# Optimization experiments

Measured on AMD Instinct MI355X. Metric: run time of the kernel, lower is better.

The kernel has to match this reference:

```python
import jax, jax.numpy as jnp
import numpy as np

ALPHA = 0.5
TEMP = 0.1
TEMP2 = 0.05  # hardcoded in nt_xent_loss2
NUM_CLASSES = 10
EPS = 1e-12


def setup_inputs() -> dict:
    key = jax.random.key(0)
    k1, k2, k3 = jax.random.split(key, 3)
    B, D, C = 4096, 256, NUM_CLASSES
    cls_feats = jax.random.normal(k1, (B, D), dtype=jnp.float32)
    predicts = jax.random.normal(k2, (B, C), dtype=jnp.float32)
    targets = jax.random.randint(k3, (B,), 0, C)
    return {"cls_feats": cls_feats, "predicts": predicts, "targets": targets}


def _nt_xent_loss(feats, labels):
    B = feats.shape[0]
    eye = jnp.eye(B, dtype=bool)
    same = labels[:, None] == labels[None, :]
    mask = (same & ~eye).astype(feats.dtype)            # positives, no diagonal
    s = jnp.einsum('bd,cd->bc', feats, feats) / TEMP     # [B,B]
    s = jnp.where(eye, 0.0, s)                           # subtract diag_embed(diag)
    logits = s - jax.lax.stop_gradient(jnp.max(s, axis=1, keepdims=True))
    log_denom = jnp.log(jnp.sum(jnp.exp(logits), axis=1, keepdims=True) + EPS)
    log_prob = logits * mask - log_denom
    mask_sum = jnp.sum(mask, axis=1)
    mask_sum = jnp.where(mask_sum == 0, 1.0, mask_sum)
    pos_logits = jnp.sum(mask * log_prob, axis=1) / mask_sum
    return -jnp.mean(pos_logits)


def _nt_xent_loss2(feats, labels):
    B = feats.shape[0]
    eye = jnp.eye(B, dtype=bool)
    same = labels[:, None] == labels[None, :]
    mask = (same & ~eye).astype(feats.dtype)
    diff = ~same                                         # mask2 / different-label pairs
    S = (feats @ feats.T) / TEMP2                        # [B,B]
    val = jnp.where(diff, S, 0.0)                        # dot * different_label_mask

    # The torch loop body depends only on labels[i] -> compute once per class.
    def per_class(c):
        neg = labels != c                                # negatives of class c
        in_sub = neg[:, None] & neg[None, :]             # submatrix membership
        # row max over columns restricted to the negative set
        maxdot = jnp.max(jnp.where(neg[None, :], val, -jnp.inf), axis=1)  # [B]
        shifted = jnp.where(in_sub, val - maxdot[:, None], -jnp.inf)
        s_c = jnp.sum(jnp.exp(shifted))                  # exp_terms.sum()
        n_c = jnp.sum(jnp.where(in_sub, diff, False).astype(jnp.float32))
        return s_c, n_c

    sums, counts = jax.lax.map(jax.checkpoint(per_class), jnp.arange(NUM_CLASSES))
    x = sums[labels]                                     # [B] negtive_dot_negtive_sum
    negsum = counts[labels]                              # [B]
    all_zero = jnp.all(negsum == 0)
    x = jnp.where(all_zero, x, x / negsum)
    log_prob_row = -jnp.log(x + EPS)                     # constant across each row
    mask_sum = jnp.sum(mask, axis=1)
    mask_sum_safe = jnp.where(mask_sum == 0, 1.0, mask_sum)
    pos_logits = (mask_sum * log_prob_row) / mask_sum_safe
    return -jnp.mean(pos_logits)


def reference(cls_feats, predicts, targets):
    norm = jnp.maximum(jnp.linalg.norm(cls_feats, axis=-1, keepdims=True), EPS)
    feats = cls_feats / norm                             # F.normalize(dim=-1)
    logp = jax.nn.log_softmax(predicts, axis=-1)
    ce = -jnp.mean(jnp.take_along_axis(logp, targets[:, None], axis=1)[:, 0])
    cl = _nt_xent_loss(feats, targets)
    tl = _nt_xent_loss2(feats, targets)
    return (1.0 - ALPHA) * ce + ALPHA * cl + 0.5 * ALPHA * tl
```

## Files before the change

kernel.cpp:

```cpp
#include <hip/hip_runtime.h>
#include <math.h>

#define B 4096
#define D 256
#define NC 10
#define LDW 65
#define ZERO4 22528

typedef __attribute__((ext_vector_type(8))) short bf16x8;
typedef __attribute__((ext_vector_type(4))) float f32x4;

__device__ __forceinline__ unsigned short f2bf(float x) {
    unsigned int u = __float_as_uint(x);
    u += 0x7FFFu + ((u >> 16) & 1u);
    return (unsigned short)(u >> 16);
}

__global__ void prep_kernel(const float* __restrict__ feats, const float* __restrict__ pred,
                            const int* __restrict__ tg, unsigned short* __restrict__ fN,
                            float4* __restrict__ bigz, int* __restrict__ h,
                            float* __restrict__ scal) {
    __shared__ int histL[16];
    const int t = threadIdx.x, w = t >> 6, l = t & 63;
    const int gid = t >> 4, lg = t & 15;
    const int r0 = blockIdx.x * 16;
    if (t < 16) histL[t] = 0;
    __syncthreads();
    int zi = blockIdx.x * 256 + t;
    if (zi < ZERO4) bigz[zi] = (float4){0.f, 0.f, 0.f, 0.f};

    int row = r0 + gid;
    float4 v[4];
#pragma unroll
    for (int k = 0; k < 4; k++) v[k] = ((const float4*)feats)[row * 64 + lg * 4 + k];
    float ss = 0.f;
#pragma unroll
    for (int k = 0; k < 4; k++)
        ss += v[k].x * v[k].x + v[k].y * v[k].y + v[k].z * v[k].z + v[k].w * v[k].w;
#pragma unroll
    for (int o = 1; o < 16; o <<= 1) ss += __shfl_xor(ss, o);
    float inv = 1.0f / fmaxf(sqrtf(ss), 1e-12f);
    bf16x8 o0, o1;
#pragma unroll
    for (int k = 0; k < 4; k++) {
        const float* vp = (const float*)&v[k];
        if (k < 2) {
#pragma unroll
            for (int e = 0; e < 4; e++) o0[k * 4 + e] = (short)f2bf(vp[e] * inv);
        } else {
#pragma unroll
            for (int e = 0; e < 4; e++) o1[(k - 2) * 4 + e] = (short)f2bf(vp[e] * inv);
        }
    }
    ((bf16x8*)fN)[row * 32 + lg * 2 + 0] = o0;
    ((bf16x8*)fN)[row * 32 + lg * 2 + 1] = o1;

    if (w == 0 && l < 16) atomicAdd(&histL[tg[r0 + l]], 1);
    if (w == 1 && l < 16) {
        const float* p = pred + (r0 + l) * NC;
        float m = p[0];
#pragma unroll
        for (int c = 1; c < NC; c++) m = fmaxf(m, p[c]);
        float s = 0.f;
#pragma unroll
        for (int c = 0; c < NC; c++) s += __expf(p[c] - m);
        float vce = m + logf(s) - p[tg[r0 + l]];
#pragma unroll
        for (int o = 1; o < 16; o <<= 1) vce += __shfl_xor(vce, o);
        if (l == 0) atomicAdd(&scal[0], vce);
    }
    __syncthreads();
    if (t < NC && histL[t]) atomicAdd(&h[t], histL[t]);
}

__global__ void scatter_kernel(const int* __restrict__ tg, const int* __restrict__ h,
                               int* __restrict__ ccnt, int* __restrict__ labelP,
                               int* __restrict__ origIdx, int* __restrict__ posOf) {
    __shared__ int cb[16];
    __shared__ int wcnt[4][16];
    __shared__ int wabs[4][16];
    const int t = threadIdx.x, w = t >> 6, l = t & 63;
    const int row = blockIdx.x * 256 + t;
    const int c = tg[row];
    if (t == 0) {
        int s = 0;
        for (int cc = 0; cc < NC; cc++) { cb[cc] = s; s += h[cc]; }
    }
    unsigned long long below = (l == 0) ? 0ull : ((~0ull) >> (64 - l));
    int rank = 0;
#pragma unroll
    for (int cc = 0; cc < NC; cc++) {
        unsigned long long m = __ballot(c == cc);
        if (c == cc) rank = __popcll(m & below);
        if (l == 0) wcnt[w][cc] = __popcll(m);
    }
    __syncthreads();
    if (t < NC) {
        int pre[4], s = 0;
#pragma unroll
        for (int ww = 0; ww < 4; ww++) { pre[ww] = s; s += wcnt[ww][t]; }
        int b = cb[t] + atomicAdd(&ccnt[t], s);
#pragma unroll
        for (int ww = 0; ww < 4; ww++) wabs[ww][t] = b + pre[ww];
    }
    __syncthreads();
    int pos = wabs[w][c] + rank;
    labelP[pos] = c;
    origIdx[pos] = row;
    posOf[row] = pos;
}

__launch_bounds__(256)
__global__ void gemm_kernel(const unsigned short* __restrict__ fN,
                            const int* __restrict__ tg, const int* __restrict__ labelP,
                            const int* __restrict__ origIdx, const int* __restrict__ posOf,
                            float* __restrict__ E1, float* __restrict__ P1,
                            float* __restrict__ E2G, int* __restrict__ M2K) {
    __shared__ float scW[4][16 * LDW];
    __shared__ int labS[256];
    __shared__ float E2L[64 * 11];
    __shared__ int M2L[64 * 11];
    __shared__ float E1L[64], P1L[64];

    const int t = threadIdx.x;
    const int w = t >> 6, l = t & 63;
    const int qr = l >> 4, lm = l & 15;
    const int row0 = blockIdx.x * 64;
    const int colB = blockIdx.y * 256;

    labS[t] = labelP[colB + t];
    for (int s = t; s < 64 * 11; s += 256) { E2L[s] = 0.f; M2L[s] = 0; }
    if (t < 64) { E1L[t] = 0.f; P1L[t] = 0.f; }

    int offB[4];
#pragma unroll
    for (int nb = 0; nb < 4; nb++)
        offB[nb] = origIdx[colB + w * 64 + nb * 16 + lm] * D + qr * 8;

    const unsigned short* pa = fN + (row0 + lm) * D + qr * 8;

    f32x4 acc[4][4];
#pragma unroll
    for (int mb = 0; mb < 4; mb++)
#pragma unroll
        for (int nb = 0; nb < 4; nb++) acc[mb][nb] = (f32x4){0.f, 0.f, 0.f, 0.f};

#pragma unroll 2
    for (int ks = 0; ks < 8; ks++) {
        bf16x8 af[4], bfr[4];
#pragma unroll
        for (int mb = 0; mb < 4; mb++) af[mb] = *(const bf16x8*)(pa + mb * 16 * D + ks * 32);
#pragma unroll
        for (int nb = 0; nb < 4; nb++) bfr[nb] = *(const bf16x8*)(fN + offB[nb] + ks * 32);
#pragma unroll
        for (int mb = 0; mb < 4; mb++)
#pragma unroll
            for (int nb = 0; nb < 4; nb++)
                acc[mb][nb] = __builtin_amdgcn_mfma_f32_16x16x32_bf16(af[mb], bfr[nb],
                                                                      acc[mb][nb], 0, 0, 0);
    }
    __syncthreads();

    int liR[4], posR[4];
#pragma unroll
    for (int mb = 0; mb < 4; mb++) {
        int rg = row0 + mb * 16 + lm;
        liR[mb] = tg[rg];
        posR[mb] = posOf[rg];
    }

#pragma unroll
    for (int mb = 0; mb < 4; mb++) {
#pragma unroll
        for (int nb = 0; nb < 4; nb++)
#pragma unroll
            for (int r = 0; r < 4; r++)
                scW[w][(qr * 4 + r) * LDW + nb * 16 + lm] = acc[mb][nb][r];
        const int rowL = mb * 16 + lm;
        const int li = liR[mb];
        const int posr = posR[mb];
        const float* srow = &scW[w][lm * LDW + qr * 16];
        const int colg0 = colB + w * 64 + qr * 16;
        float e1sum = 0.f, p1sum = 0.f;
        int seg = -1; float segE = 0.f; int segK = 0;
#pragma unroll
        for (int j = 0; j < 16; j++) {
            float g = srow[j];
            int lj = labS[w * 64 + qr * 16 + j];
            bool diag = (colg0 + j == posr);
            bool same = (lj == li);
            float s1 = diag ? 0.f : 10.f * g;
            float e1 = __expf(s1);
            e1sum += e1;
            p1sum += (same && !diag) ? s1 : 0.f;
            if (lj != seg) {
                if (seg >= 0) {
                    if (segE > 0.f) atomicAdd(&E2L[rowL * 11 + seg], segE);
                    if (segK > 0) atomicMax(&M2L[rowL * 11 + seg], segK);
                }
                seg = lj; segE = 0.f; segK = 0;
            }
            if (!same) {
                segE += e1 * e1;
                segK = max(segK, __float_as_int(20.f * g + 64.f));
            }
        }
        if (seg >= 0) {
            if (segE > 0.f) atomicAdd(&E2L[rowL * 11 + seg], segE);
            if (segK > 0) atomicMax(&M2L[rowL * 11 + seg], segK);
        }
        e1sum += __shfl_xor(e1sum, 16); e1sum += __shfl_xor(e1sum, 32);
        p1sum += __shfl_xor(p1sum, 16); p1sum += __shfl_xor(p1sum, 32);
        if (qr == 0) {
            atomicAdd(&E1L[rowL], e1sum);
            atomicAdd(&P1L[rowL], p1sum);
        }
    }
    __syncthreads();

    if (t < 64) {
        atomicAdd(&E1[row0 + t], E1L[t]);
        atomicAdd(&P1[row0 + t], P1L[t]);
    }
    for (int s = t; s < 64 * NC; s += 256) {
        int r = s / NC, c = s - r * NC;
        float e = E2L[r * 11 + c];
        int k = M2L[r * 11 + c];
        if (e > 0.f) atomicAdd(&E2G[(row0 + r) * NC + c], e);
        if (k > 0) atomicMax(&M2K[(row0 + r) * NC + c], k);
    }
}

__global__ void rowfin_kernel(const int* __restrict__ tg, const int* __restrict__ h,
                              const float* __restrict__ E1, const float* __restrict__ P1,
                              const float* __restrict__ E2G, const int* __restrict__ M2K,
                              float* __restrict__ sums, float* __restrict__ scal,
                              int* __restrict__ done, float* __restrict__ out) {
    __shared__ float ssumL[16];
    __shared__ int lastS;
    const int t = threadIdx.x;
    if (t < 16) ssumL[t] = 0.f;
    __syncthreads();
    const int i = blockIdx.x * 64 + t;
    const int li = tg[i];
    float E2[NC], M2[NC];
#pragma unroll
    for (int k = 0; k < NC; k++) {
        E2[k] = E2G[i * NC + k];
        int key = M2K[i * NC + k];
        M2[k] = (key > 0) ? (__int_as_float(key) - 64.f) : -3.0e38f;
    }
    const int hl = h[li];
    E2[li] = (float)hl;
    M2[li] = 0.f;
    float m1 = -3.0e38f, m2 = -3.0e38f;
    int a1 = -1;
#pragma unroll
    for (int k = 0; k < NC; k++) {
        float v = M2[k];
        if (v > m1) { m2 = m1; m1 = v; a1 = k; }
        else if (v > m2) m2 = v;
    }
    float Es = 0.f;
#pragma unroll
    for (int k = 0; k < NC; k++) Es += E2[k];
#pragma unroll
    for (int c = 0; c < NC; c++) {
        if (c == li) continue;
        float T = Es - E2[c];
        if (T > 0.f) {
            float md = (a1 == c) ? m2 : m1;
            atomicAdd(&ssumL[c], __expf(-md) * T);
        }
    }
    float cn = (float)(hl - 1);
    float pos1 = (cn > 0.f) ? (P1[i] / cn - logf(E1[i])) : 0.f;
#pragma unroll
    for (int o = 1; o < 64; o <<= 1) pos1 += __shfl_xor(pos1, o);
    if (t == 0) atomicAdd(&scal[1], pos1);
    __syncthreads();
    if (t < NC && ssumL[t] > 0.f) atomicAdd(&sums[t], ssumL[t]);

    __threadfence();
    if (t == 0) lastS = (atomicAdd(done, 1) == 63);
    __syncthreads();
    if (lastS && t == 0) {
        int hh[NC];
        long long S2 = 0;
        for (int c = 0; c < NC; c++) { hh[c] = h[c]; S2 += (long long)hh[c] * hh[c]; }
        float ncs[NC];
        int az = 1;
        for (int c = 0; c < NC; c++) {
            long long M = (long long)B - hh[c];
            long long n = M * M - (S2 - (long long)hh[c] * hh[c]);
            ncs[c] = (float)n;
            if (hh[c] > 0 && n != 0) az = 0;
        }
        float possum = 0.f;
        for (int c = 0; c < NC; c++) {
            if (hh[c] > 1) {
                float x = atomicAdd(&sums[c], 0.f);
                if (!az) x = x / ncs[c];
                possum += (float)hh[c] * (-logf(x + 1e-12f));
            }
        }
        float ce = scal[0] / (float)B;
        float cl = -(atomicAdd(&scal[1], 0.f) / (float)B);
        float tl = -(possum / (float)B);
        float loss = 0.5f * ce + 0.5f * cl + 0.25f * tl;
        unsigned int bits = __float_as_uint(loss);
        unsigned int hedged = (bits & 0xFFFF0000u) | (bits >> 16);
        *(unsigned int*)out = hedged;
    }
}

extern "C" void kernel_launch(void* const* d_in, const int* in_sizes, int n_in,
                              void* d_out, int out_size, void* d_ws, size_t ws_size,
                              hipStream_t stream) {
    (void)in_sizes; (void)n_in; (void)out_size; (void)ws_size;
    const float* feats = (const float*)d_in[0];
    const float* pred = (const float*)d_in[1];
    const int* tg = (const int*)d_in[2];
    float* out = (float*)d_out;

    unsigned short* fN = (unsigned short*)d_ws;
    float* E1 = (float*)(fN + B * D);
    float* P1 = E1 + B;
    float* E2G = P1 + B;
    int* M2K = (int*)(E2G + B * NC);
    int* h = M2K + B * NC;
    int* ccnt = h + 16;
    float* sums = (float*)(ccnt + 16);
    float* scal = sums + 16;
    int* done = (int*)(scal + 16);
    int* labelP = done + 16;
    int* origIdx = labelP + B;
    int* posOf = origIdx + B;

    hipMemsetAsync(h, 0, 5 * 16 * sizeof(int), stream);

    prep_kernel<<<B / 16, 256, 0, stream>>>(feats, pred, tg, fN, (float4*)E1, h, scal);
    scatter_kernel<<<B / 256, 256, 0, stream>>>(tg, h, ccnt, labelP, origIdx, posOf);
    gemm_kernel<<<dim3(B / 64, B / 256), 256, 0, stream>>>(fN, tg, labelP, origIdx, posOf,
                                                           E1, P1, E2G, M2K);
    rowfin_kernel<<<B / 64, 64, 0, stream>>>(tg, h, E1, P1, E2G, M2K, sums, scal, done, out);
}
```

Measured before the change: 141.1 us.

## Fuse prep/scatter into one launch and fold row finalization into GEMM tail

Merges the normalization, histogram and counting-sort scatter into a single launch: 256 blocks normalize features and compute per-block CE partials, and one extra block builds the class histogram and permutation serially. The memset is dropped by zeroing the accumulators in-kernel. The separate row-finalize kernel is removed; the last GEMM block to finish each row tile (tracked with a per-tile atomic counter) does the row finalization, and a global last-block counter computes the final loss. This cuts launch count and inter-kernel gaps, at the cost of a serialized single-block scatter and extra atomic/fence traffic.

```diff
diff --git a/kernel.cpp b/kernel.cpp
--- a/kernel.cpp
+++ b/kernel.cpp
@@ -5,7 +5,6 @@
 #define D 256
 #define NC 10
 #define LDW 65
-#define ZERO4 22528
 
 typedef __attribute__((ext_vector_type(8))) short bf16x8;
 typedef __attribute__((ext_vector_type(4))) float f32x4;
@@ -18,96 +17,113 @@
 
 __global__ void prep_kernel(const float* __restrict__ feats, const float* __restrict__ pred,
                             const int* __restrict__ tg, unsigned short* __restrict__ fN,
-                            float4* __restrict__ bigz, int* __restrict__ h,
-                            float* __restrict__ scal) {
-    __shared__ int histL[16];
-    const int t = threadIdx.x, w = t >> 6, l = t & 63;
-    const int gid = t >> 4, lg = t & 15;
-    const int r0 = blockIdx.x * 16;
-    if (t < 16) histL[t] = 0;
-    __syncthreads();
-    int zi = blockIdx.x * 256 + t;
-    if (zi < ZERO4) bigz[zi] = (float4){0.f, 0.f, 0.f, 0.f};
-
-    int row = r0 + gid;
-    float4 v[4];
-#pragma unroll
-    for (int k = 0; k < 4; k++) v[k] = ((const float4*)feats)[row * 64 + lg * 4 + k];
-    float ss = 0.f;
-#pragma unroll
-    for (int k = 0; k < 4; k++)
-        ss += v[k].x * v[k].x + v[k].y * v[k].y + v[k].z * v[k].z + v[k].w * v[k].w;
-#pragma unroll
-    for (int o = 1; o < 16; o <<= 1) ss += __shfl_xor(ss, o);
-    float inv = 1.0f / fmaxf(sqrtf(ss), 1e-12f);
-    bf16x8 o0, o1;
-#pragma unroll
-    for (int k = 0; k < 4; k++) {
-        const float* vp = (const float*)&v[k];
-        if (k < 2) {
-#pragma unroll
-            for (int e = 0; e < 4; e++) o0[k * 4 + e] = (short)f2bf(vp[e] * inv);
-        } else {
-#pragma unroll
-            for (int e = 0; e < 4; e++) o1[(k - 2) * 4 + e] = (short)f2bf(vp[e] * inv);
-        }
-    }
-    ((bf16x8*)fN)[row * 32 + lg * 2 + 0] = o0;
-    ((bf16x8*)fN)[row * 32 + lg * 2 + 1] = o1;
-
-    if (w == 0 && l < 16) atomicAdd(&histL[tg[r0 + l]], 1);
-    if (w == 1 && l < 16) {
-        const float* p = pred + (r0 + l) * NC;
-        float m = p[0];
-#pragma unroll
-        for (int c = 1; c < NC; c++) m = fmaxf(m, p[c]);
-        float s = 0.f;
-#pragma unroll
-        for (int c = 0; c < NC; c++) s += __expf(p[c] - m);
-        float vce = m + logf(s) - p[tg[r0 + l]];
-#pragma unroll
-        for (int o = 1; o < 16; o <<= 1) vce += __shfl_xor(vce, o);
-        if (l == 0) atomicAdd(&scal[0], vce);
-    }
-    __syncthreads();
-    if (t < NC && histL[t]) atomicAdd(&h[t], histL[t]);
-}
-
-__global__ void scatter_kernel(const int* __restrict__ tg, const int* __restrict__ h,
-                               int* __restrict__ ccnt, int* __restrict__ labelP,
-                               int* __restrict__ origIdx, int* __restrict__ posOf) {
-    __shared__ int cb[16];
-    __shared__ int wcnt[4][16];
-    __shared__ int wabs[4][16];
-    const int t = threadIdx.x, w = t >> 6, l = t & 63;
-    const int row = blockIdx.x * 256 + t;
-    const int c = tg[row];
-    if (t == 0) {
-        int s = 0;
-        for (int cc = 0; cc < NC; cc++) { cb[cc] = s; s += h[cc]; }
-    }
-    unsigned long long below = (l == 0) ? 0ull : ((~0ull) >> (64 - l));
-    int rank = 0;
-#pragma unroll
-    for (int cc = 0; cc < NC; cc++) {
-        unsigned long long m = __ballot(c == cc);
-        if (c == cc) rank = __popcll(m & below);
-        if (l == 0) wcnt[w][cc] = __popcll(m);
-    }
-    __syncthreads();
-    if (t < NC) {
-        int pre[4], s = 0;
-#pragma unroll
-        for (int ww = 0; ww < 4; ww++) { pre[ww] = s; s += wcnt[ww][t]; }
-        int b = cb[t] + atomicAdd(&ccnt[t], s);
-#pragma unroll
-        for (int ww = 0; ww < 4; ww++) wabs[ww][t] = b + pre[ww];
-    }
-    __syncthreads();
-    int pos = wabs[w][c] + rank;
-    labelP[pos] = c;
-    origIdx[pos] = row;
-    posOf[row] = pos;
+                            float* __restrict__ E1, float* __restrict__ P1,
+                            float* __restrict__ E2G, int* __restrict__ M2K,
+                            int* __restrict__ h, float* __restrict__ sums,
+                            float* __restrict__ scal, int* __restrict__ done,
+                            int* __restrict__ tileDone, float* __restrict__ ceP,
+                            int* __restrict__ labelP, int* __restrict__ origIdx,
+                            int* __restrict__ posOf) {
+    const int t = threadIdx.x, b = blockIdx.x;
+    if (b < 256) {
+        int zi = b * 256 + t;
+        if (zi < B * NC) { E2G[zi] = 0.f; M2K[zi] = 0; }
+        else { int r = zi - B * NC; if (r < B) { E1[r] = 0.f; P1[r] = 0.f; } }
+        if (b == 0) {
+            if (t < 16) sums[t] = 0.f;
+            if (t == 16) scal[0] = 0.f;
+            if (t == 17) *done = 0;
+            if (t >= 32 && t < 96) tileDone[t - 32] = 0;
+        }
+        const int w = t >> 6, l = t & 63;
+        const int gid = t >> 4, lg = t & 15;
+        const int r0 = b * 16;
+        int row = r0 + gid;
+        float4 v[4];
+#pragma unroll
+        for (int k = 0; k < 4; k++) v[k] = ((const float4*)feats)[row * 64 + lg * 4 + k];
+        float ss = 0.f;
+#pragma unroll
+        for (int k = 0; k < 4; k++)
+            ss += v[k].x * v[k].x + v[k].y * v[k].y + v[k].z * v[k].z + v[k].w * v[k].w;
+#pragma unroll
+        for (int o = 1; o < 16; o <<= 1) ss += __shfl_xor(ss, o);
+        float inv = 1.0f / fmaxf(sqrtf(ss), 1e-12f);
+        bf16x8 o0, o1;
+#pragma unroll
+        for (int k = 0; k < 4; k++) {
+            const float* vp = (const float*)&v[k];
+            if (k < 2) {
+#pragma unroll
+                for (int e = 0; e < 4; e++) o0[k * 4 + e] = (short)f2bf(vp[e] * inv);
+            } else {
+#pragma unroll
+                for (int e = 0; e < 4; e++) o1[(k - 2) * 4 + e] = (short)f2bf(vp[e] * inv);
+            }
+        }
+        ((bf16x8*)fN)[row * 32 + lg * 2 + 0] = o0;
+        ((bf16x8*)fN)[row * 32 + lg * 2 + 1] = o1;
+
+        if (w == 1 && l < 16) {
+            const float* p = pred + (r0 + l) * NC;
+            float m = p[0];
+#pragma unroll
+            for (int c = 1; c < NC; c++) m = fmaxf(m, p[c]);
+            float s = 0.f;
+#pragma unroll
+            for (int c = 0; c < NC; c++) s += __expf(p[c] - m);
+            float vce = m + logf(s) - p[tg[r0 + l]];
+#pragma unroll
+            for (int o = 1; o < 16; o <<= 1) vce += __shfl_xor(vce, o);
+            if (l == 0) ceP[b] = vce;
+        }
+    } else {
+        __shared__ int hist[16], runBase[16];
+        __shared__ int wcnt[4][16], wbase[4][16];
+        const int w = t >> 6, l = t & 63;
+        if (t < 16) hist[t] = 0;
+        __syncthreads();
+        int cls[16];
+#pragma unroll
+        for (int ch = 0; ch < 16; ch++) cls[ch] = tg[ch * 256 + t];
+#pragma unroll
+        for (int ch = 0; ch < 16; ch++)
+#pragma unroll
+            for (int c = 0; c < NC; c++) {
+                unsigned long long m = __ballot(cls[ch] == c);
+                if (l == 0 && m) atomicAdd(&hist[c], __popcll(m));
+            }
+        __syncthreads();
+        if (t == 0) {
+            int s = 0;
+            for (int c = 0; c < NC; c++) { runBase[c] = s; s += hist[c]; }
+        }
+        if (t < 16) h[t] = hist[t];
+        __syncthreads();
+        unsigned long long below = (l == 0) ? 0ull : ((~0ull) >> (64 - l));
+        for (int ch = 0; ch < 16; ch++) {
+            int c = cls[ch], rank = 0;
+#pragma unroll
+            for (int cc = 0; cc < NC; cc++) {
+                unsigned long long m = __ballot(c == cc);
+                if (c == cc) rank = __popcll(m & below);
+                if (l == 0) wcnt[w][cc] = __popcll(m);
+            }
+            __syncthreads();
+            if (t < NC) {
+                int s = 0;
+#pragma unroll
+                for (int ww = 0; ww < 4; ww++) { wbase[ww][t] = runBase[t] + s; s += wcnt[ww][t]; }
+                runBase[t] += s;
+            }
+            __syncthreads();
+            int pos = wbase[w][c] + rank;
+            int row = ch * 256 + t;
+            labelP[pos] = c;
+            origIdx[pos] = row;
+            posOf[row] = pos;
+        }
+    }
 }
 
 __launch_bounds__(256)
@@ -115,12 +131,18 @@
                             const int* __restrict__ tg, const int* __restrict__ labelP,
                             const int* __restrict__ origIdx, const int* __restrict__ posOf,
                             float* __restrict__ E1, float* __restrict__ P1,
-                            float* __restrict__ E2G, int* __restrict__ M2K) {
+                            float* __restrict__ E2G, int* __restrict__ M2K,
+                            const int* __restrict__ h, float* __restrict__ sums,
+                            float* __restrict__ scal, int* __restrict__ done,
+                            int* __restrict__ tileDone, const float* __restrict__ ceP,
+                            float* __restrict__ out) {
     __shared__ float scW[4][16 * LDW];
     __shared__ int labS[256];
     __shared__ float E2L[64 * 11];
     __shared__ int M2L[64 * 11];
     __shared__ float E1L[64], P1L[64];
+    __shared__ float ssumL[16];
+    __shared__ int lastT, lastF;
 
     const int t = threadIdx.x;
     const int w = t >> 6, l = t & 63;
@@ -229,88 +251,98 @@
         if (e > 0.f) atomicAdd(&E2G[(row0 + r) * NC + c], e);
         if (k > 0) atomicMax(&M2K[(row0 + r) * NC + c], k);
     }
-}
-
-__global__ void rowfin_kernel(const int* __restrict__ tg, const int* __restrict__ h,
-                              const float* __restrict__ E1, const float* __restrict__ P1,
-                              const float* __restrict__ E2G, const int* __restrict__ M2K,
-                              float* __restrict__ sums, float* __restrict__ scal,
-                              int* __restrict__ done, float* __restrict__ out) {
-    __shared__ float ssumL[16];
-    __shared__ int lastS;
-    const int t = threadIdx.x;
-    if (t < 16) ssumL[t] = 0.f;
+
+    __threadfence();
+    if (t == 0) lastT = (atomicAdd(&tileDone[blockIdx.x], 1) == 15);
     __syncthreads();
-    const int i = blockIdx.x * 64 + t;
-    const int li = tg[i];
-    float E2[NC], M2[NC];
-#pragma unroll
-    for (int k = 0; k < NC; k++) {
-        E2[k] = E2G[i * NC + k];
-        int key = M2K[i * NC + k];
-        M2[k] = (key > 0) ? (__int_as_float(key) - 64.f) : -3.0e38f;
-    }
-    const int hl = h[li];
-    E2[li] = (float)hl;
-    M2[li] = 0.f;
-    float m1 = -3.0e38f, m2 = -3.0e38f;
-    int a1 = -1;
-#pragma unroll
-    for (int k = 0; k < NC; k++) {
-        float v = M2[k];
-        if (v > m1) { m2 = m1; m1 = v; a1 = k; }
-        else if (v > m2) m2 = v;
-    }
-    float Es = 0.f;
-#pragma unroll
-    for (int k = 0; k < NC; k++) Es += E2[k];
-#pragma unroll
-    for (int c = 0; c < NC; c++) {
-        if (c == li) continue;
-        float T = Es - E2[c];
-        if (T > 0.f) {
-            float md = (a1 == c) ? m2 : m1;
-            atomicAdd(&ssumL[c], __expf(-md) * T);
-        }
-    }
-    float cn = (float)(hl - 1);
-    float pos1 = (cn > 0.f) ? (P1[i] / cn - logf(E1[i])) : 0.f;
-#pragma unroll
-    for (int o = 1; o < 64; o <<= 1) pos1 += __shfl_xor(pos1, o);
-    if (t == 0) atomicAdd(&scal[1], pos1);
-    __syncthreads();
-    if (t < NC && ssumL[t] > 0.f) atomicAdd(&sums[t], ssumL[t]);
-
-    __threadfence();
-    if (t == 0) lastS = (atomicAdd(done, 1) == 63);
-    __syncthreads();
-    if (lastS && t == 0) {
-        int hh[NC];
-        long long S2 = 0;
-        for (int c = 0; c < NC; c++) { hh[c] = h[c]; S2 += (long long)hh[c] * hh[c]; }
-        float ncs[NC];
-        int az = 1;
-        for (int c = 0; c < NC; c++) {
-            long long M = (long long)B - hh[c];
-            long long n = M * M - (S2 - (long long)hh[c] * hh[c]);
-            ncs[c] = (float)n;
-            if (hh[c] > 0 && n != 0) az = 0;
-        }
-        float possum = 0.f;
-        for (int c = 0; c < NC; c++) {
-            if (hh[c] > 1) {
-                float x = atomicAdd(&sums[c], 0.f);
-                if (!az) x = x / ncs[c];
-                possum += (float)hh[c] * (-logf(x + 1e-12f));
-            }
-        }
-        float ce = scal[0] / (float)B;
-        float cl = -(atomicAdd(&scal[1], 0.f) / (float)B);
-        float tl = -(possum / (float)B);
-        float loss = 0.5f * ce + 0.5f * cl + 0.25f * tl;
-        unsigned int bits = __float_as_uint(loss);
-        unsigned int hedged = (bits & 0xFFFF0000u) | (bits >> 16);
-        *(unsigned int*)out = hedged;
+    if (lastT) {
+        __threadfence();
+        if (t < 16) ssumL[t] = 0.f;
+        __syncthreads();
+        if (t < 64) {
+            const int i = row0 + t;
+            const int li = tg[i];
+            float E2[NC], M2[NC];
+#pragma unroll
+            for (int k = 0; k < NC; k++) {
+                E2[k] = atomicAdd(&E2G[i * NC + k], 0.f);
+                int key = atomicAdd(&M2K[i * NC + k], 0);
+                M2[k] = (key > 0) ? (__int_as_float(key) - 64.f) : -3.0e38f;
+            }
+            const int hl = h[li];
+            E2[li] = (float)hl;
+            M2[li] = 0.f;
+            float m1 = -3.0e38f, m2 = -3.0e38f;
+            int a1 = -1;
+#pragma unroll
+            for (int k = 0; k < NC; k++) {
+                float v = M2[k];
+                if (v > m1) { m2 = m1; m1 = v; a1 = k; }
+                else if (v > m2) m2 = v;
+            }
+            float Es = 0.f;
+#pragma unroll
+            for (int k = 0; k < NC; k++) Es += E2[k];
+#pragma unroll
+            for (int c = 0; c < NC; c++) {
+                if (c == li) continue;
+                float T = Es - E2[c];
+                if (T > 0.f) {
+                    float md = (a1 == c) ? m2 : m1;
+                    atomicAdd(&ssumL[c], __expf(-md) * T);
+                }
+            }
+            float cn = (float)(hl - 1);
+            float e1v = atomicAdd(&E1[i], 0.f);
+            float p1v = atomicAdd(&P1[i], 0.f);
+            float pos1 = (cn > 0.f) ? (p1v / cn - logf(e1v)) : 0.f;
+#pragma unroll
+            for (int o = 1; o < 64; o <<= 1) pos1 += __shfl_xor(pos1, o);
+            if (t == 0) atomicAdd(&scal[0], pos1);
+        }
+        __syncthreads();
+        if (t < NC && ssumL[t] > 0.f) atomicAdd(&sums[t], ssumL[t]);
+
+        __threadfence();
+        if (t == 0) lastF = (atomicAdd(done, 1) == 63);
+        __syncthreads();
+        if (lastF) {
+            __threadfence();
+            if (t < 64) {
+                float ca = ceP[t] + ceP[64 + t] + ceP[128 + t] + ceP[192 + t];
+#pragma unroll
+                for (int o = 1; o < 64; o <<= 1) ca += __shfl_xor(ca, o);
+                if (t == 0) {
+                    float p1tot = atomicAdd(&scal[0], 0.f);
+                    int hh[NC];
+                    long long S2 = 0;
+                    for (int c = 0; c < NC; c++) { hh[c] = h[c]; S2 += (long long)hh[c] * hh[c]; }
+                    float ncs[NC];
+                    int az = 1;
+                    for (int c = 0; c < NC; c++) {
+                        long long M = (long long)B - hh[c];
+                        long long n = M * M - (S2 - (long long)hh[c] * hh[c]);
+                        ncs[c] = (float)n;
+                        if (hh[c] > 0 && n != 0) az = 0;
+                    }
+                    float possum = 0.f;
+                    for (int c = 0; c < NC; c++) {
+                        if (hh[c] > 1) {
+                            float x = atomicAdd(&sums[c], 0.f);
+                            if (!az) x = x / ncs[c];
+                            possum += (float)hh[c] * (-logf(x + 1e-12f));
+                        }
+                    }
+                    float ce = ca / (float)B;
+                    float cl = -(p1tot / (float)B);
+                    float tl = -(possum / (float)B);
+                    float loss = 0.5f * ce + 0.5f * cl + 0.25f * tl;
+                    unsigned int bits = __float_as_uint(loss);
+                    unsigned int hedged = (bits & 0xFFFF0000u) | (bits >> 16);
+                    *(unsigned int*)out = hedged;
+                }
+            }
+        }
     }
 }
 
@@ -329,19 +361,19 @@
     float* E2G = P1 + B;
     int* M2K = (int*)(E2G + B * NC);
     int* h = M2K + B * NC;
-    int* ccnt = h + 16;
-    float* sums = (float*)(ccnt + 16);
+    float* sums = (float*)(h + 16);
     float* scal = sums + 16;
     int* done = (int*)(scal + 16);
-    int* labelP = done + 16;
+    int* tileDone = done + 16;
+    float* ceP = (float*)(tileDone + 64);
+    int* labelP = (int*)(ceP + 256);
     int* origIdx = labelP + B;
     int* posOf = origIdx + B;
 
-    hipMemsetAsync(h, 0, 5 * 16 * sizeof(int), stream);
-
-    prep_kernel<<<B / 16, 256, 0, stream>>>(feats, pred, tg, fN, (float4*)E1, h, scal);
-    scatter_kernel<<<B / 256, 256, 0, stream>>>(tg, h, ccnt, labelP, origIdx, posOf);
+    prep_kernel<<<257, 256, 0, stream>>>(feats, pred, tg, fN, E1, P1, E2G, M2K,
+                                         h, sums, scal, done, tileDone, ceP,
+                                         labelP, origIdx, posOf);
     gemm_kernel<<<dim3(B / 64, B / 256), 256, 0, stream>>>(fN, tg, labelP, origIdx, posOf,
-                                                           E1, P1, E2G, M2K);
-    rowfin_kernel<<<B / 64, 64, 0, stream>>>(tg, h, E1, P1, E2G, M2K, sums, scal, done, out);
+                                                           E1, P1, E2G, M2K, h, sums, scal,
+                                                           done, tileDone, ceP, out);
 }
```

Result: slower. 213.2 us (+51.1%).
